# Kernel tuning notes

Hardware: AMD Instinct MI355X
Metric: run time of the kernel (lower is better)

## Reference

```python
import jax, jax.numpy as jnp
import numpy as np

N = 50000      # num nodes
E = 800000     # num edges (before self loops)
HID = 64       # hidden_channels
HEADS = 4
B = 256        # num graphs in batch
TEXT, VIS, AUD = 768, 512, 128


def setup_inputs() -> dict:
    key = jax.random.key(0)
    ks = jax.random.split(key, 24)
    rn = lambda k, shape: jax.random.normal(k, shape, dtype=jnp.float32) * 0.05
    inp = {}
    inp["x"] = jax.random.normal(ks[0], (N, TEXT), dtype=jnp.float32)
    inp["node_type"] = jax.random.randint(ks[1], (N,), 0, 3, dtype=jnp.int32)
    inp["edge_index"] = jax.random.randint(ks[2], (2, E), 0, N, dtype=jnp.int32)
    inp["batch"] = jnp.sort(jax.random.randint(ks[3], (N,), 0, B, dtype=jnp.int32))
    # modality projections
    inp["Wt"] = rn(ks[4], (TEXT, HID)); inp["bt"] = jnp.zeros((HID,), jnp.float32)
    inp["Wv"] = rn(ks[5], (VIS, HID));  inp["bv"] = jnp.zeros((HID,), jnp.float32)
    inp["Wa"] = rn(ks[6], (AUD, HID));  inp["ba"] = jnp.zeros((HID,), jnp.float32)
    # GATConv1: in=HID, out=HID, heads=HEADS, concat=True
    inp["W1"]  = rn(ks[7], (HID, HEADS * HID))
    inp["a1s"] = rn(ks[8], (HEADS, HID))
    inp["a1d"] = rn(ks[9], (HEADS, HID))
    inp["b1"]  = jnp.zeros((HEADS * HID,), jnp.float32)
    # GATConv2: in=HID*HEADS, out=HID, heads=1, concat=False
    inp["W2"]  = rn(ks[10], (HID * HEADS, HID))
    inp["a2s"] = rn(ks[11], (1, HID))
    inp["a2d"] = rn(ks[12], (1, HID))
    inp["b2"]  = jnp.zeros((HID,), jnp.float32)
    # final classifier (num_classes==2 -> out_dim 1, squeezed)
    inp["Wl"] = rn(ks[13], (HID, 1)); inp["bl"] = jnp.zeros((1,), jnp.float32)
    return inp


def gat_conv(x, edge_index, W, a_src, a_dst, bias, concat):
    """PyG-style GATConv (eval mode, add_self_loops=True, shared lin for src/dst)."""
    n = x.shape[0]
    heads, c = a_src.shape
    loops = jnp.arange(n, dtype=edge_index.dtype)
    src = jnp.concatenate([edge_index[0], loops])
    dst = jnp.concatenate([edge_index[1], loops])
    h = (x @ W).reshape(n, heads, c)                       # [N, H, C]
    alpha_s = jnp.einsum('nhc,hc->nh', h, a_src)           # [N, H]
    alpha_d = jnp.einsum('nhc,hc->nh', h, a_dst)
    e = jax.nn.leaky_relu(alpha_s[src] + alpha_d[dst], 0.2)  # [E', H]
    # numerically-stable softmax over incoming edges of each dst node
    m = jax.ops.segment_max(e, dst, num_segments=n)
    e = jnp.exp(e - m[dst])
    denom = jax.ops.segment_sum(e, dst, num_segments=n)
    alpha = e / (denom[dst] + 1e-16)                        # [E', H]
    out = jax.ops.segment_sum(h[src] * alpha[:, :, None], dst, num_segments=n)
    out = out.reshape(n, heads * c) if concat else out.mean(axis=1)
    return out + bias


def reference(x, node_type, edge_index, batch,
              Wt, bt, Wv, bv, Wa, ba,
              W1, a1s, a1d, b1, W2, a2s, a2d, b2, Wl, bl):
    # masked multimodal projection (type 0=text, 1=vision, 2=audio)
    t = x[:, :TEXT] @ Wt + bt
    v = x[:, :VIS] @ Wv + bv
    a = x[:, :AUD] @ Wa + ba
    nt = node_type[:, None]
    h = jnp.where(nt == 0, t, jnp.where(nt == 1, v, a))     # [N, HID]
    h = jax.nn.elu(gat_conv(h, edge_index, W1, a1s, a1d, b1, concat=True))
    h = gat_conv(h, edge_index, W2, a2s, a2d, b2, concat=False)  # [N, HID]
    # global mean pool over graphs
    sums = jax.ops.segment_sum(h, batch, num_segments=B)
    cnts = jax.ops.segment_sum(jnp.ones((h.shape[0], 1), h.dtype), batch, num_segments=B)
    g = sums / jnp.maximum(cnts, 1.0)                       # [B, HID]
    out = (g @ Wl + bl).squeeze(-1)                          # [B] (binary logit)
    return out
```

## Files before the change

### kernel.cpp

```cpp
#include <hip/hip_runtime.h>
#include <cstdint>
#include <cstddef>

#define TEXTD 768
#define VISD  512
#define AUDD  128

__device__ __forceinline__ float wred_sum(float v){
  #pragma unroll
  for (int m = 32; m >= 1; m >>= 1) v += __shfl_xor(v, m, 64);
  return v;
}
__device__ __forceinline__ float wred_max(float v){
  #pragma unroll
  for (int m = 32; m >= 1; m >>= 1) v = fmaxf(v, __shfl_xor(v, m, 64));
  return v;
}

__global__ __launch_bounds__(256) void k_bcount(const int* __restrict__ ntype, int nN, int nblk,
                                                int* __restrict__ bcnt){
  int b = blockIdx.x;
  int i = b*256 + threadIdx.x;
  int lane = threadIdx.x & 63, w = threadIdx.x >> 6;
  int ty = (i < nN) ? ntype[i] : -1;
  __shared__ int wc[4][3];
  #pragma unroll
  for (int t = 0; t < 3; t++){
    unsigned long long m = __ballot(ty == t);
    if (lane == 0) wc[w][t] = __popcll(m);
  }
  __syncthreads();
  if (threadIdx.x < 3){
    int t = threadIdx.x;
    bcnt[t*nblk + b] = wc[0][t] + wc[1][t] + wc[2][t] + wc[3][t];
  }
}
__global__ __launch_bounds__(1024) void k_bscan(const int* __restrict__ bcnt, int nblk, int nN,
                                                int* __restrict__ boff, int* __restrict__ toff,
                                                int* __restrict__ tcnt){
  __shared__ int s[2048];
  int n3 = nblk*3;
  int t = threadIdx.x;
  for (int i = t; i < n3; i += 1024) s[i] = bcnt[i];
  __syncthreads();
  if (t == 0){
    int run = 0;
    for (int i = 0; i < n3; i++){ int v = s[i]; s[i] = run; run += v; }
  }
  __syncthreads();
  for (int i = t; i < n3; i += 1024) boff[i] = s[i];
  if (t == 0){
    toff[0] = 0;         toff[1] = s[nblk];           toff[2] = s[2*nblk];
    tcnt[0] = s[nblk];   tcnt[1] = s[2*nblk]-s[nblk]; tcnt[2] = nN - s[2*nblk];
  }
}
__global__ __launch_bounds__(256) void k_bscatter(const int* __restrict__ ntype, int nN, int nblk,
                                                  const int* __restrict__ boff, int* __restrict__ order){
  int b = blockIdx.x;
  int i = b*256 + threadIdx.x;
  int lane = threadIdx.x & 63, w = threadIdx.x >> 6;
  int ty = (i < nN) ? ntype[i] : -1;
  __shared__ int wc[4][3];
  __shared__ int woff[4][3];
  unsigned long long masks[3];
  #pragma unroll
  for (int t = 0; t < 3; t++){
    masks[t] = __ballot(ty == t);
    if (lane == 0) wc[w][t] = __popcll(masks[t]);
  }
  __syncthreads();
  if (threadIdx.x < 3){
    int t = threadIdx.x, run = 0;
    #pragma unroll
    for (int ww = 0; ww < 4; ww++){ woff[ww][t] = run; run += wc[ww][t]; }
  }
  __syncthreads();
  if (ty >= 0){
    int r = __popcll(masks[ty] & ((1ULL << lane) - 1ULL));
    int pos = boff[ty*nblk + b] + woff[w][ty] + r;
    order[pos] = i;
  }
}

__global__ __launch_bounds__(256) void k_projgemm(const float* __restrict__ x,
    const int* __restrict__ order, const int* __restrict__ toff, const int* __restrict__ tcnt,
    const float* __restrict__ Wt, const float* __restrict__ bt,
    const float* __restrict__ Wv, const float* __restrict__ bv,
    const float* __restrict__ Wa, const float* __restrict__ ba,
    float* __restrict__ h0){
  int ty = blockIdx.y;
  int cnt = tcnt[ty];
  int tile = blockIdx.x;
  if (tile*64 >= cnt) return;
  const float* W; const float* bias; int dim;
  if (ty == 0)      { W = Wt; bias = bt; dim = TEXTD; }
  else if (ty == 1) { W = Wv; bias = bv; dim = VISD; }
  else              { W = Wa; bias = ba; dim = AUDD; }
  int off = toff[ty];

  __shared__ float xsT[64][68];
  __shared__ float ws [64][68];
  __shared__ int   nid[64];

  int t = threadIdx.x;
  if (t < 64){
    int idx = tile*64 + t;
    nid[t] = (idx < cnt) ? order[off + idx] : -1;
  }
  __syncthreads();

  int node_l = t & 63;
  int ndl = nid[node_l];
  const float* xrow = x + (size_t)(ndl < 0 ? 0 : ndl) * TEXTD;
  int wrow = t >> 2, wu = t & 3;
  int wvq  = t >> 6;
  int n0 = (t & 15)*4, c0 = (t >> 4)*4;
  float acc[4][4] = {};

  for (int k0 = 0; k0 < dim; k0 += 64){
    __syncthreads();
    #pragma unroll
    for (int j = 0; j < 4; j++){
      int f4 = wvq*4 + j;
      float4 v = *reinterpret_cast<const float4*>(xrow + k0 + f4*4);
      xsT[f4*4+0][node_l] = v.x;
      xsT[f4*4+1][node_l] = v.y;
      xsT[f4*4+2][node_l] = v.z;
      xsT[f4*4+3][node_l] = v.w;
    }
    #pragma unroll
    for (int j = 0; j < 4; j++){
      int f4 = j*4 + wu;
      float4 v = *reinterpret_cast<const float4*>(W + (size_t)(k0 + wrow)*64 + f4*4);
      *reinterpret_cast<float4*>(&ws[wrow][f4*4]) = v;
    }
    __syncthreads();
    #pragma unroll 8
    for (int kk = 0; kk < 64; kk++){
      float4 xv = *reinterpret_cast<const float4*>(&xsT[kk][n0]);
      float4 wv = *reinterpret_cast<const float4*>(&ws[kk][c0]);
      float xa[4] = {xv.x, xv.y, xv.z, xv.w};
      float wb[4] = {wv.x, wv.y, wv.z, wv.w};
      #pragma unroll
      for (int i = 0; i < 4; i++)
        #pragma unroll
        for (int j = 0; j < 4; j++)
          acc[i][j] += xa[i] * wb[j];
    }
  }

  float4 b4 = *reinterpret_cast<const float4*>(bias + c0);
  float bb[4] = {b4.x, b4.y, b4.z, b4.w};
  #pragma unroll
  for (int i = 0; i < 4; i++){
    int nd = nid[n0 + i];
    if (nd >= 0){
      float4 o4 = make_float4(acc[i][0]+bb[0], acc[i][1]+bb[1], acc[i][2]+bb[2], acc[i][3]+bb[3]);
      *reinterpret_cast<float4*>(h0 + (size_t)nd*64 + c0) = o4;
    }
  }
}

__global__ void k_deg_init(int* __restrict__ deg, int nN){
  int i = blockIdx.x*blockDim.x + threadIdx.x;
  if (i < nN) deg[i] = 1;
}
__global__ void k_deg_edges(const int* __restrict__ ei, int E, int* __restrict__ deg){
  int i = blockIdx.x*blockDim.x + threadIdx.x;
  if (i < E) atomicAdd(&deg[ei[E + i]], 1);
}
__global__ __launch_bounds__(1024) void k_scan(const int* __restrict__ deg, int* __restrict__ off, int n){
  __shared__ int wsum[16];
  __shared__ int carry_s;
  int t = threadIdx.x, lane = t & 63, w = t >> 6;
  if (t == 0) carry_s = 0;
  __syncthreads();
  for (int base = 0; base < n; base += 1024){
    int i = base + t;
    int v = (i < n) ? deg[i] : 0;
    int orig = v;
    #pragma unroll
    for (int o = 1; o < 64; o <<= 1){ int u = __shfl_up(v, o, 64); if (lane >= o) v += u; }
    if (lane == 63) wsum[w] = v;
    __syncthreads();
    if (t < 16){
      int xv = wsum[t];
      #pragma unroll
      for (int o = 1; o < 16; o <<= 1){ int u = __shfl_up(xv, o, 16); if (t >= o) xv += u; }
      wsum[t] = xv;
    }
    __syncthreads();
    int wbase = (w == 0) ? 0 : wsum[w-1];
    int incl = v + wbase;
    int carry = carry_s;
    if (i < n) off[i] = carry + incl - orig;
    __syncthreads();
    if (t == 0) carry_s = carry + wsum[15];
    __syncthreads();
  }
  if (threadIdx.x == 0) off[n] = carry_s;
}
__global__ void k_pos_copy(const int* __restrict__ off, int* __restrict__ pos, int nN){
  int i = blockIdx.x*blockDim.x + threadIdx.x;
  if (i < nN) pos[i] = off[i];
}
__global__ void k_scatter(const int* __restrict__ ei, int E, int nN,
                          int* __restrict__ pos, int* __restrict__ csr_src){
  int i = blockIdx.x*blockDim.x + threadIdx.x;
  int total = E + nN;
  if (i >= total) return;
  int s, d;
  if (i < E){ s = ei[i]; d = ei[E + i]; } else { s = i - E; d = s; }
  int p = atomicAdd(&pos[d], 1);
  csr_src[p] = s;
}

__global__ __launch_bounds__(256) void k_afold(const float* __restrict__ W1,
    const float* __restrict__ a1s, const float* __restrict__ a1d,
    float* __restrict__ wfs, float* __restrict__ wfd){
  int t = threadIdx.x;
  int k = t & 63, h = t >> 6;
  const float* wr = W1 + (size_t)k*256 + h*64;
  const float* as = a1s + h*64;
  const float* ad = a1d + h*64;
  float s = 0.f, d = 0.f;
  for (int c = 0; c < 64; c += 4){
    float4 w  = *reinterpret_cast<const float4*>(wr + c);
    float4 sa = *reinterpret_cast<const float4*>(as + c);
    float4 da = *reinterpret_cast<const float4*>(ad + c);
    s += w.x*sa.x + w.y*sa.y + w.z*sa.z + w.w*sa.w;
    d += w.x*da.x + w.y*da.y + w.z*da.z + w.w*da.w;
  }
  wfs[k*4 + h] = s;
  wfd[k*4 + h] = d;
}

__global__ __launch_bounds__(256) void k_alpha1(const float* __restrict__ h0,
    const float* __restrict__ wfs, const float* __restrict__ wfd,
    float* __restrict__ as1, float* __restrict__ ad1, int nN){
  __shared__ float xsT[64][68];
  __shared__ float sW[64][8];
  int t = threadIdx.x;
  int base = blockIdx.x*64;
  int row = t >> 2, fq = t & 3;
  {
    int nd = base + row; if (nd >= nN) nd = nN - 1;
    const float* hr = h0 + (size_t)nd*64;
    #pragma unroll
    for (int j = 0; j < 4; j++){
      int f4 = j*4 + fq;
      float4 v = *reinterpret_cast<const float4*>(hr + f4*4);
      xsT[f4*4+0][row] = v.x; xsT[f4*4+1][row] = v.y;
      xsT[f4*4+2][row] = v.z; xsT[f4*4+3][row] = v.w;
    }
  }
  if (t < 64){
    float4 s4 = *reinterpret_cast<const float4*>(wfs + t*4);
    float4 d4 = *reinterpret_cast<const float4*>(wfd + t*4);
    sW[t][0]=s4.x; sW[t][1]=s4.y; sW[t][2]=s4.z; sW[t][3]=s4.w;
    sW[t][4]=d4.x; sW[t][5]=d4.y; sW[t][6]=d4.z; sW[t][7]=d4.w;
  }
  __syncthreads();
  int node = t >> 2, h = t & 3;
  float s = 0.f, d = 0.f;
  #pragma unroll 8
  for (int k = 0; k < 64; k++){
    float xv = xsT[k][node];
    s += xv * sW[k][h];
    d += xv * sW[k][h+4];
  }
  int nd = base + node;
  if (nd < nN){ as1[nd*4 + h] = s; ad1[nd*4 + h] = d; }
}

__global__ __launch_bounds__(64) void k_gat1z(const int* __restrict__ off, const int* __restrict__ srcs,
    const float* __restrict__ as1, const float* __restrict__ ad1,
    const float* __restrict__ h0, float* __restrict__ z, int nN){
  int n = blockIdx.x;
  int L = threadIdx.x;
  int hL = L >> 4, c4 = (L & 15)*4;
  __shared__ int   s_src[64];
  __shared__ float s_p[64][4];
  float ad[4];
  { float4 a = *reinterpret_cast<const float4*>(ad1 + (size_t)n*4);
    ad[0]=a.x; ad[1]=a.y; ad[2]=a.z; ad[3]=a.w; }
  int s0 = off[n], s1 = off[n+1];
  float m[4] = {-1e30f,-1e30f,-1e30f,-1e30f};
  float den[4] = {0.f,0.f,0.f,0.f};
  float4 acc = make_float4(0.f,0.f,0.f,0.f);
  for (int base = s0; base < s1; base += 64){
    int e = base + L;
    int cl = min(64, s1 - base);
    bool valid = (e < s1);
    int sv = 0; float v[4];
    if (valid){
      sv = srcs[e];
      float4 a = *reinterpret_cast<const float4*>(as1 + (size_t)sv*4);
      float av[4] = {a.x,a.y,a.z,a.w};
      #pragma unroll
      for (int h = 0; h < 4; h++){ float tt = av[h] + ad[h]; v[h] = (tt>0.f)?tt:0.2f*tt; }
    } else {
      #pragma unroll
      for (int h = 0; h < 4; h++) v[h] = -1e30f;
    }
    float sc[4];
    #pragma unroll
    for (int h = 0; h < 4; h++){
      float cm = wred_max(v[h]);
      float mn = fmaxf(m[h], cm);
      sc[h] = __expf(m[h] - mn);
      m[h] = mn;
      float p = valid ? __expf(v[h] - mn) : 0.f;
      den[h] = den[h]*sc[h] + wred_sum(p);
      if (valid) s_p[L][h] = p;
    }
    { float s4 = sc[hL]; acc.x*=s4; acc.y*=s4; acc.z*=s4; acc.w*=s4; }
    if (valid) s_src[L] = sv;
    __syncthreads();
    #pragma unroll 4
    for (int e2 = 0; e2 < cl; e2++){
      int sr = s_src[e2];
      float pp = s_p[e2][hL];
      float4 hv = *reinterpret_cast<const float4*>(h0 + (size_t)sr*64 + c4);
      acc.x += pp*hv.x; acc.y += pp*hv.y; acc.z += pp*hv.z; acc.w += pp*hv.w;
    }
    __syncthreads();
  }
  float dl = den[hL] + 1e-16f;
  *reinterpret_cast<float4*>(z + (size_t)n*256 + hL*64 + c4) =
      make_float4(acc.x/dl, acc.y/dl, acc.z/dl, acc.w/dl);
}

__global__ __launch_bounds__(256) void k_glin1(const float* __restrict__ z,
    const float* __restrict__ W1, const float* __restrict__ b1,
    float* __restrict__ g1, int nN){
  int tile = blockIdx.x, q = blockIdx.y;
  int base = tile*64;
  __shared__ float xsT[64][68];
  __shared__ float ws [64][68];
  int t = threadIdx.x;
  int row = t >> 2, fq = t & 3;
  {
    int nd = base + row; if (nd >= nN) nd = nN - 1;
    const float* zr = z + (size_t)nd*256 + q*64;
    #pragma unroll
    for (int j = 0; j < 4; j++){
      int f4 = j*4 + fq;
      float4 v = *reinterpret_cast<const float4*>(zr + f4*4);
      xsT[f4*4+0][row] = v.x; xsT[f4*4+1][row] = v.y;
      xsT[f4*4+2][row] = v.z; xsT[f4*4+3][row] = v.w;
    }
  }
  #pragma unroll
  for (int j = 0; j < 4; j++){
    int f4 = j*4 + fq;
    float4 v = *reinterpret_cast<const float4*>(W1 + (size_t)row*256 + q*64 + f4*4);
    *reinterpret_cast<float4*>(&ws[row][f4*4]) = v;
  }
  __syncthreads();

  int n0 = (t & 15)*4, c0 = (t >> 4)*4;
  float acc[4][4] = {};
  #pragma unroll 8
  for (int k = 0; k < 64; k++){
    float4 xv = *reinterpret_cast<const float4*>(&xsT[k][n0]);
    float4 wv = *reinterpret_cast<const float4*>(&ws[k][c0]);
    float xa[4] = {xv.x, xv.y, xv.z, xv.w};
    float wb[4] = {wv.x, wv.y, wv.z, wv.w};
    #pragma unroll
    for (int i = 0; i < 4; i++)
      #pragma unroll
      for (int j = 0; j < 4; j++)
        acc[i][j] += xa[i] * wb[j];
  }
  float4 b4 = *reinterpret_cast<const float4*>(b1 + q*64 + c0);
  float bb[4] = {b4.x, b4.y, b4.z, b4.w};
  #pragma unroll
  for (int i = 0; i < 4; i++){
    int nd = base + n0 + i;
    if (nd < nN){
      float o[4];
      #pragma unroll
      for (int j = 0; j < 4; j++){
        float u = acc[i][j] + bb[j];
        o[j] = (u > 0.f) ? u : expm1f(u);
      }
      *reinterpret_cast<float4*>(g1 + (size_t)nd*256 + q*64 + c0) =
          make_float4(o[0], o[1], o[2], o[3]);
    }
  }
}

__global__ __launch_bounds__(256) void k_lin2t(const float* __restrict__ g1,
    const float* __restrict__ W2, const float* __restrict__ a2s, const float* __restrict__ a2d,
    float* __restrict__ h2, float* __restrict__ as2, float* __restrict__ ad2, int nN){
  int tile = blockIdx.x;
  int base = tile*64;
  __shared__ float xsT[64][68];
  __shared__ float ws [64][68];
  __shared__ float sPart[16][64];
  __shared__ float dPart[16][64];

  int t = threadIdx.x;
  int row = t >> 2, fq = t & 3;
  int ndl = base + row; if (ndl >= nN) ndl = nN - 1;
  const float* gr = g1 + (size_t)ndl*256;
  int n0 = (t & 15)*4, c0 = (t >> 4)*4, qg = t >> 4;
  float acc[4][4] = {};

  for (int k0 = 0; k0 < 256; k0 += 64){
    __syncthreads();
    #pragma unroll
    for (int j = 0; j < 4; j++){
      int f4 = j*4 + fq;
      float4 v = *reinterpret_cast<const float4*>(gr + k0 + f4*4);
      xsT[f4*4+0][row] = v.x; xsT[f4*4+1][row] = v.y;
      xsT[f4*4+2][row] = v.z; xsT[f4*4+3][row] = v.w;
    }
    #pragma unroll
    for (int j = 0; j < 4; j++){
      int f4 = j*4 + fq;
      float4 v = *reinterpret_cast<const float4*>(W2 + (size_t)(k0 + row)*64 + f4*4);
      *reinterpret_cast<float4*>(&ws[row][f4*4]) = v;
    }
    __syncthreads();
    #pragma unroll 8
    for (int k = 0; k < 64; k++){
      float4 xv = *reinterpret_cast<const float4*>(&xsT[k][n0]);
      float4 wv = *reinterpret_cast<const float4*>(&ws[k][c0]);
      float xa[4] = {xv.x, xv.y, xv.z, xv.w};
      float wb[4] = {wv.x, wv.y, wv.z, wv.w};
      #pragma unroll
      for (int i = 0; i < 4; i++)
        #pragma unroll
        for (int j = 0; j < 4; j++)
          acc[i][j] += xa[i] * wb[j];
    }
  }

  float avs[4], avd[4];
  {
    float4 s4 = *reinterpret_cast<const float4*>(a2s + c0);
    float4 d4 = *reinterpret_cast<const float4*>(a2d + c0);
    avs[0]=s4.x; avs[1]=s4.y; avs[2]=s4.z; avs[3]=s4.w;
    avd[0]=d4.x; avd[1]=d4.y; avd[2]=d4.z; avd[3]=d4.w;
  }
  #pragma unroll
  for (int i = 0; i < 4; i++){
    int nd = base + n0 + i;
    float sp = acc[i][0]*avs[0] + acc[i][1]*avs[1] + acc[i][2]*avs[2] + acc[i][3]*avs[3];
    float dp = acc[i][0]*avd[0] + acc[i][1]*avd[1] + acc[i][2]*avd[2] + acc[i][3]*avd[3];
    sPart[qg][n0+i] = sp;
    dPart[qg][n0+i] = dp;
    if (nd < nN){
      float4 o4 = make_float4(acc[i][0], acc[i][1], acc[i][2], acc[i][3]);
      *reinterpret_cast<float4*>(h2 + (size_t)nd*64 + c0) = o4;
    }
  }
  __syncthreads();
  if (t < 64){
    int nd = base + t;
    if (nd < nN){
      float s = 0.f, d = 0.f;
      #pragma unroll
      for (int g = 0; g < 16; g++){ s += sPart[g][t]; d += dPart[g][t]; }
      as2[nd] = s;
      ad2[nd] = d;
    }
  }
}

__global__ __launch_bounds__(256) void k_gat2v(const int* __restrict__ off, const int* __restrict__ srcs,
    const float* __restrict__ as2, const float* __restrict__ ad2,
    const float* __restrict__ h2, const float* __restrict__ b2,
    float* __restrict__ g2, int nN){
  int w = threadIdx.x >> 6, L = threadIdx.x & 63;
  int n = blockIdx.x*4 + w;
  if (n >= nN) return;
  int g = L >> 4, c4 = (L & 15)*4;
  float ad = ad2[n];
  int s0 = off[n], s1 = off[n+1];
  float m = -1e30f, den = 0.f;
  float4 acc = make_float4(0.f,0.f,0.f,0.f);
  for (int base = s0; base < s1; base += 64){
    int e = base + L;
    int cl = min(64, s1 - base);
    bool valid = (e < s1);
    int sv = 0; float v = -1e30f;
    if (valid){
      sv = srcs[e];
      float tt = as2[sv] + ad;
      v = (tt>0.f)?tt:0.2f*tt;
    }
    float cm = wred_max(v);
    float mn = fmaxf(m, cm);
    float sc = __expf(m - mn);
    m = mn;
    float p = valid ? __expf(v - mn) : 0.f;
    den = den*sc + wred_sum(p);
    acc.x*=sc; acc.y*=sc; acc.z*=sc; acc.w*=sc;
    int iters = (cl + 3) >> 2;
    for (int it = 0; it < iters; ++it){
      int e2   = it*4 + g;
      int esrc = (e2 < cl) ? e2 : (cl - 1);
      int   sr = __shfl(sv, esrc, 64);
      float pp = __shfl(p,  esrc, 64);
      if (e2 < cl){
        float4 hv = *reinterpret_cast<const float4*>(h2 + (size_t)sr*64 + c4);
        acc.x += pp*hv.x; acc.y += pp*hv.y; acc.z += pp*hv.z; acc.w += pp*hv.w;
      }
    }
  }
  #pragma unroll
  for (int s = 16; s <= 32; s <<= 1){
    acc.x += __shfl_xor(acc.x, s, 64);
    acc.y += __shfl_xor(acc.y, s, 64);
    acc.z += __shfl_xor(acc.z, s, 64);
    acc.w += __shfl_xor(acc.w, s, 64);
  }
  float dl = den + 1e-16f;
  if (L < 16){
    float4 b4 = *reinterpret_cast<const float4*>(b2 + c4);
    float4 o4 = make_float4(acc.x/dl + b4.x, acc.y/dl + b4.y,
                            acc.z/dl + b4.z, acc.w/dl + b4.w);
    *reinterpret_cast<float4*>(g2 + (size_t)n*64 + c4) = o4;
  }
}

__global__ void k_bstart(const int* __restrict__ batch, int nN, int B, int* __restrict__ bstart){
  int i = blockIdx.x*blockDim.x + threadIdx.x;
  if (i < nN){
    int prev = (i == 0) ? -1 : batch[i-1];
    int cur  = batch[i];
    for (int b = prev+1; b <= cur; b++) bstart[b] = i;
  } else if (i == nN){
    int last = batch[nN-1];
    for (int b = last+1; b <= B; b++) bstart[b] = nN;
  }
}

__global__ __launch_bounds__(64) void k_pool(const float* __restrict__ g2, const int* __restrict__ bstart,
    const float* __restrict__ Wl, const float* __restrict__ bl, float* __restrict__ out, int B){
  int b = blockIdx.x, c = threadIdx.x;
  int r0 = bstart[b], r1 = bstart[b+1];
  float s = 0.f;
  int i = r0;
  for (; i + 4 <= r1; i += 4){
    s += g2[(size_t)(i+0)*64 + c];
    s += g2[(size_t)(i+1)*64 + c];
    s += g2[(size_t)(i+2)*64 + c];
    s += g2[(size_t)(i+3)*64 + c];
  }
  for (; i < r1; i++) s += g2[(size_t)i*64 + c];
  float g = s / fmaxf((float)(r1 - r0), 1.f);
  float v = wred_sum(g * Wl[c]);
  if (c == 0) out[b] = v + bl[0];
}

extern "C" void kernel_launch(void* const* d_in, const int* in_sizes, int n_in,
                              void* d_out, int out_size, void* d_ws, size_t ws_size,
                              hipStream_t stream){
  const float* x    = (const float*)d_in[0];
  const int*   ntyp = (const int*)  d_in[1];
  const int*   ei   = (const int*)  d_in[2];
  const int*   batch= (const int*)  d_in[3];
  const float* Wt = (const float*)d_in[4];
  const float* bt = (const float*)d_in[5];
  const float* Wv = (const float*)d_in[6];
  const float* bv = (const float*)d_in[7];
  const float* Wa = (const float*)d_in[8];
  const float* ba = (const float*)d_in[9];
  const float* W1 = (const float*)d_in[10];
  const float* a1s= (const float*)d_in[11];
  const float* a1d= (const float*)d_in[12];
  const float* b1 = (const float*)d_in[13];
  const float* W2 = (const float*)d_in[14];
  const float* a2s= (const float*)d_in[15];
  const float* a2d= (const float*)d_in[16];
  const float* b2 = (const float*)d_in[17];
  const float* Wl = (const float*)d_in[18];
  const float* bl = (const float*)d_in[19];

  const int N = in_sizes[1];
  const int E = in_sizes[2] / 2;
  const int B = out_size;
  const int nblk = (N + 255)/256;

  char* ws = (char*)d_ws;
  size_t o = 0;
  auto alloc = [&](size_t bytes) -> void* {
    void* p = ws + o;
    o = (o + bytes + 255) & ~(size_t)255;
    return p;
  };
  int*   csr_off = (int*)  alloc((size_t)(N+1)*4);
  int*   pos     = (int*)  alloc((size_t)N*4);
  int*   csr_src = (int*)  alloc((size_t)(E+N)*4);
  float* as1     = (float*)alloc((size_t)N*4*4);
  float* ad1     = (float*)alloc((size_t)N*4*4);
  float* h0      = (float*)alloc((size_t)N*64*4);
  float* zbuf    = (float*)alloc((size_t)N*256*4);
  float* g1      = (float*)alloc((size_t)N*256*4);
  int*   bstart  = (int*)  alloc((size_t)(B+1)*4);
  int*   bcnt    = (int*)  alloc((size_t)nblk*3*4);
  int*   boff    = (int*)  alloc((size_t)nblk*3*4);
  int*   toff    = (int*)  alloc(3*4);
  int*   tcnt    = (int*)  alloc(3*4);
  int*   order   = (int*)  alloc((size_t)N*4);
  float* wfs     = (float*)alloc(256*4);
  float* wfd     = (float*)alloc(256*4);
  float* h2  = h0;
  float* as2 = as1;
  float* ad2 = ad1;
  float* g2  = zbuf;

  k_bcount  <<<nblk, 256, 0, stream>>>(ntyp, N, nblk, bcnt);
  k_bscan   <<<1, 1024, 0, stream>>>(bcnt, nblk, N, boff, toff, tcnt);
  k_bscatter<<<nblk, 256, 0, stream>>>(ntyp, N, nblk, boff, order);

  k_deg_init <<<(N + 255)/256, 256, 0, stream>>>(pos, N);
  k_deg_edges<<<(E + 255)/256, 256, 0, stream>>>(ei, E, pos);
  k_scan     <<<1, 1024, 0, stream>>>(pos, csr_off, N);
  k_pos_copy <<<(N + 255)/256, 256, 0, stream>>>(csr_off, pos, N);
  k_scatter  <<<(E + N + 255)/256, 256, 0, stream>>>(ei, E, N, pos, csr_src);

  k_bstart<<<(N + 1 + 255)/256, 256, 0, stream>>>(batch, N, B, bstart);

  k_afold<<<1, 256, 0, stream>>>(W1, a1s, a1d, wfs, wfd);

  {
    dim3 g((N + 63)/64, 3);
    k_projgemm<<<g, 256, 0, stream>>>(x, order, toff, tcnt, Wt, bt, Wv, bv, Wa, ba, h0);
  }

  k_alpha1<<<(N + 63)/64, 256, 0, stream>>>(h0, wfs, wfd, as1, ad1, N);
  k_gat1z <<<N, 64, 0, stream>>>(csr_off, csr_src, as1, ad1, h0, zbuf, N);
  {
    dim3 g((N + 63)/64, 4);
    k_glin1<<<g, 256, 0, stream>>>(zbuf, W1, b1, g1, N);
  }

  k_lin2t<<<(N + 63)/64, 256, 0, stream>>>(g1, W2, a2s, a2d, h2, as2, ad2, N);
  k_gat2v<<<(N + 3)/4, 256, 0, stream>>>(csr_off, csr_src, as2, ad2, h2, b2, g2, N);
  k_pool<<<B, 64, 0, stream>>>(g2, bstart, Wl, bl, (float*)d_out, B);
}
```

Measured before the change: 386.6 us.

## Fuse attention logits into projection GEMM, merge setup kernels, batch GAT1 nodes per block

Computes layer-1 source and destination attention logits in the projection GEMM epilogue, using a shared-memory partial reduction, so the separate k_alpha1 pass and its reread of h0 go away. Degree initialisation moves into k_bcount, and the scan now writes the scatter cursor directly, which removes two small kernel launches. k_gat1z now processes four nodes per 256-thread block, one wavefront per node, with per-wave shared buffers and no block barriers. The wave-local shared-memory handoff relies on wavefront lockstep execution, and the GEMM epilogue adds shared-memory traffic and a serial 64-thread reduction.

```diff
diff --git a/kernel.cpp b/kernel.cpp
--- a/kernel.cpp
+++ b/kernel.cpp
@@ -18,11 +18,12 @@
 }
 
 __global__ __launch_bounds__(256) void k_bcount(const int* __restrict__ ntype, int nN, int nblk,
-                                                int* __restrict__ bcnt){
+                                                int* __restrict__ bcnt, int* __restrict__ deg){
   int b = blockIdx.x;
   int i = b*256 + threadIdx.x;
   int lane = threadIdx.x & 63, w = threadIdx.x >> 6;
   int ty = (i < nN) ? ntype[i] : -1;
+  if (i < nN) deg[i] = 1;
   __shared__ int wc[4][3];
   #pragma unroll
   for (int t = 0; t < 3; t++){
@@ -82,94 +83,11 @@
   }
 }
 
-__global__ __launch_bounds__(256) void k_projgemm(const float* __restrict__ x,
-    const int* __restrict__ order, const int* __restrict__ toff, const int* __restrict__ tcnt,
-    const float* __restrict__ Wt, const float* __restrict__ bt,
-    const float* __restrict__ Wv, const float* __restrict__ bv,
-    const float* __restrict__ Wa, const float* __restrict__ ba,
-    float* __restrict__ h0){
-  int ty = blockIdx.y;
-  int cnt = tcnt[ty];
-  int tile = blockIdx.x;
-  if (tile*64 >= cnt) return;
-  const float* W; const float* bias; int dim;
-  if (ty == 0)      { W = Wt; bias = bt; dim = TEXTD; }
-  else if (ty == 1) { W = Wv; bias = bv; dim = VISD; }
-  else              { W = Wa; bias = ba; dim = AUDD; }
-  int off = toff[ty];
-
-  __shared__ float xsT[64][68];
-  __shared__ float ws [64][68];
-  __shared__ int   nid[64];
-
-  int t = threadIdx.x;
-  if (t < 64){
-    int idx = tile*64 + t;
-    nid[t] = (idx < cnt) ? order[off + idx] : -1;
-  }
-  __syncthreads();
-
-  int node_l = t & 63;
-  int ndl = nid[node_l];
-  const float* xrow = x + (size_t)(ndl < 0 ? 0 : ndl) * TEXTD;
-  int wrow = t >> 2, wu = t & 3;
-  int wvq  = t >> 6;
-  int n0 = (t & 15)*4, c0 = (t >> 4)*4;
-  float acc[4][4] = {};
-
-  for (int k0 = 0; k0 < dim; k0 += 64){
-    __syncthreads();
-    #pragma unroll
-    for (int j = 0; j < 4; j++){
-      int f4 = wvq*4 + j;
-      float4 v = *reinterpret_cast<const float4*>(xrow + k0 + f4*4);
-      xsT[f4*4+0][node_l] = v.x;
-      xsT[f4*4+1][node_l] = v.y;
-      xsT[f4*4+2][node_l] = v.z;
-      xsT[f4*4+3][node_l] = v.w;
-    }
-    #pragma unroll
-    for (int j = 0; j < 4; j++){
-      int f4 = j*4 + wu;
-      float4 v = *reinterpret_cast<const float4*>(W + (size_t)(k0 + wrow)*64 + f4*4);
-      *reinterpret_cast<float4*>(&ws[wrow][f4*4]) = v;
-    }
-    __syncthreads();
-    #pragma unroll 8
-    for (int kk = 0; kk < 64; kk++){
-      float4 xv = *reinterpret_cast<const float4*>(&xsT[kk][n0]);
-      float4 wv = *reinterpret_cast<const float4*>(&ws[kk][c0]);
-      float xa[4] = {xv.x, xv.y, xv.z, xv.w};
-      float wb[4] = {wv.x, wv.y, wv.z, wv.w};
-      #pragma unroll
-      for (int i = 0; i < 4; i++)
-        #pragma unroll
-        for (int j = 0; j < 4; j++)
-          acc[i][j] += xa[i] * wb[j];
-    }
-  }
-
-  float4 b4 = *reinterpret_cast<const float4*>(bias + c0);
-  float bb[4] = {b4.x, b4.y, b4.z, b4.w};
-  #pragma unroll
-  for (int i = 0; i < 4; i++){
-    int nd = nid[n0 + i];
-    if (nd >= 0){
-      float4 o4 = make_float4(acc[i][0]+bb[0], acc[i][1]+bb[1], acc[i][2]+bb[2], acc[i][3]+bb[3]);
-      *reinterpret_cast<float4*>(h0 + (size_t)nd*64 + c0) = o4;
-    }
-  }
-}
-
-__global__ void k_deg_init(int* __restrict__ deg, int nN){
-  int i = blockIdx.x*blockDim.x + threadIdx.x;
-  if (i < nN) deg[i] = 1;
-}
 __global__ void k_deg_edges(const int* __restrict__ ei, int E, int* __restrict__ deg){
   int i = blockIdx.x*blockDim.x + threadIdx.x;
   if (i < E) atomicAdd(&deg[ei[E + i]], 1);
 }
-__global__ __launch_bounds__(1024) void k_scan(const int* __restrict__ deg, int* __restrict__ off, int n){
+__global__ __launch_bounds__(1024) void k_scan(int* __restrict__ deg, int* __restrict__ off, int n){
   __shared__ int wsum[16];
   __shared__ int carry_s;
   int t = threadIdx.x, lane = t & 63, w = t >> 6;
@@ -193,16 +111,12 @@
     int wbase = (w == 0) ? 0 : wsum[w-1];
     int incl = v + wbase;
     int carry = carry_s;
-    if (i < n) off[i] = carry + incl - orig;
+    if (i < n){ int e = carry + incl - orig; off[i] = e; deg[i] = e; }
     __syncthreads();
     if (t == 0) carry_s = carry + wsum[15];
     __syncthreads();
   }
   if (threadIdx.x == 0) off[n] = carry_s;
-}
-__global__ void k_pos_copy(const int* __restrict__ off, int* __restrict__ pos, int nN){
-  int i = blockIdx.x*blockDim.x + threadIdx.x;
-  if (i < nN) pos[i] = off[i];
 }
 __global__ void k_scatter(const int* __restrict__ ei, int E, int nN,
                           int* __restrict__ pos, int* __restrict__ csr_src){
@@ -235,52 +149,139 @@
   wfd[k*4 + h] = d;
 }
 
-__global__ __launch_bounds__(256) void k_alpha1(const float* __restrict__ h0,
+__global__ __launch_bounds__(256) void k_projgemm(const float* __restrict__ x,
+    const int* __restrict__ order, const int* __restrict__ toff, const int* __restrict__ tcnt,
+    const float* __restrict__ Wt, const float* __restrict__ bt,
+    const float* __restrict__ Wv, const float* __restrict__ bv,
+    const float* __restrict__ Wa, const float* __restrict__ ba,
     const float* __restrict__ wfs, const float* __restrict__ wfd,
-    float* __restrict__ as1, float* __restrict__ ad1, int nN){
+    float* __restrict__ h0, float* __restrict__ as1, float* __restrict__ ad1){
+  int ty = blockIdx.y;
+  int cnt = tcnt[ty];
+  int tile = blockIdx.x;
+  if (tile*64 >= cnt) return;
+  const float* W; const float* bias; int dim;
+  if (ty == 0)      { W = Wt; bias = bt; dim = TEXTD; }
+  else if (ty == 1) { W = Wv; bias = bv; dim = VISD; }
+  else              { W = Wa; bias = ba; dim = AUDD; }
+  int off = toff[ty];
+
   __shared__ float xsT[64][68];
-  __shared__ float sW[64][8];
+  __shared__ float ws [64][68];
+  __shared__ int   nid[64];
+
   int t = threadIdx.x;
-  int base = blockIdx.x*64;
-  int row = t >> 2, fq = t & 3;
-  {
-    int nd = base + row; if (nd >= nN) nd = nN - 1;
-    const float* hr = h0 + (size_t)nd*64;
+  if (t < 64){
+    int idx = tile*64 + t;
+    nid[t] = (idx < cnt) ? order[off + idx] : -1;
+  }
+  __syncthreads();
+
+  int node_l = t & 63;
+  int ndl = nid[node_l];
+  const float* xrow = x + (size_t)(ndl < 0 ? 0 : ndl) * TEXTD;
+  int wrow = t >> 2, wu = t & 3;
+  int wvq  = t >> 6;
+  int n0 = (t & 15)*4, c0 = (t >> 4)*4, qg = t >> 4;
+  float acc[4][4] = {};
+
+  for (int k0 = 0; k0 < dim; k0 += 64){
+    __syncthreads();
     #pragma unroll
     for (int j = 0; j < 4; j++){
-      int f4 = j*4 + fq;
-      float4 v = *reinterpret_cast<const float4*>(hr + f4*4);
-      xsT[f4*4+0][row] = v.x; xsT[f4*4+1][row] = v.y;
-      xsT[f4*4+2][row] = v.z; xsT[f4*4+3][row] = v.w;
-    }
-  }
+      int f4 = wvq*4 + j;
+      float4 v = *reinterpret_cast<const float4*>(xrow + k0 + f4*4);
+      xsT[f4*4+0][node_l] = v.x;
+      xsT[f4*4+1][node_l] = v.y;
+      xsT[f4*4+2][node_l] = v.z;
+      xsT[f4*4+3][node_l] = v.w;
+    }
+    #pragma unroll
+    for (int j = 0; j < 4; j++){
+      int f4 = j*4 + wu;
+      float4 v = *reinterpret_cast<const float4*>(W + (size_t)(k0 + wrow)*64 + f4*4);
+      *reinterpret_cast<float4*>(&ws[wrow][f4*4]) = v;
+    }
+    __syncthreads();
+    #pragma unroll 8
+    for (int kk = 0; kk < 64; kk++){
+      float4 xv = *reinterpret_cast<const float4*>(&xsT[kk][n0]);
+      float4 wv = *reinterpret_cast<const float4*>(&ws[kk][c0]);
+      float xa[4] = {xv.x, xv.y, xv.z, xv.w};
+      float wb[4] = {wv.x, wv.y, wv.z, wv.w};
+      #pragma unroll
+      for (int i = 0; i < 4; i++)
+        #pragma unroll
+        for (int j = 0; j < 4; j++)
+          acc[i][j] += xa[i] * wb[j];
+    }
+  }
+
+  float4 b4 = *reinterpret_cast<const float4*>(bias + c0);
+  float bb[4] = {b4.x, b4.y, b4.z, b4.w};
+  #pragma unroll
+  for (int i = 0; i < 4; i++){
+    int nd = nid[n0 + i];
+    if (nd >= 0){
+      float4 o4 = make_float4(acc[i][0]+bb[0], acc[i][1]+bb[1], acc[i][2]+bb[2], acc[i][3]+bb[3]);
+      *reinterpret_cast<float4*>(h0 + (size_t)nd*64 + c0) = o4;
+    }
+  }
+
+  __syncthreads();
+  float* spart = &ws [0][0];
+  float* dpart = &xsT[0][0];
+  float4 wsv[4], wdv[4];
+  #pragma unroll
+  for (int j = 0; j < 4; j++){
+    wsv[j] = *reinterpret_cast<const float4*>(wfs + (c0+j)*4);
+    wdv[j] = *reinterpret_cast<const float4*>(wfd + (c0+j)*4);
+  }
+  #pragma unroll
+  for (int i = 0; i < 4; i++){
+    float hv[4];
+    #pragma unroll
+    for (int j = 0; j < 4; j++) hv[j] = acc[i][j] + bb[j];
+    float s0v = hv[0]*wsv[0].x + hv[1]*wsv[1].x + hv[2]*wsv[2].x + hv[3]*wsv[3].x;
+    float s1v = hv[0]*wsv[0].y + hv[1]*wsv[1].y + hv[2]*wsv[2].y + hv[3]*wsv[3].y;
+    float s2v = hv[0]*wsv[0].z + hv[1]*wsv[1].z + hv[2]*wsv[2].z + hv[3]*wsv[3].z;
+    float s3v = hv[0]*wsv[0].w + hv[1]*wsv[1].w + hv[2]*wsv[2].w + hv[3]*wsv[3].w;
+    float d0v = hv[0]*wdv[0].x + hv[1]*wdv[1].x + hv[2]*wdv[2].x + hv[3]*wdv[3].x;
+    float d1v = hv[0]*wdv[0].y + hv[1]*wdv[1].y + hv[2]*wdv[2].y + hv[3]*wdv[3].y;
+    float d2v = hv[0]*wdv[0].z + hv[1]*wdv[1].z + hv[2]*wdv[2].z + hv[3]*wdv[3].z;
+    float d3v = hv[0]*wdv[0].w + hv[1]*wdv[1].w + hv[2]*wdv[2].w + hv[3]*wdv[3].w;
+    int nidx = (n0 + i)*64 + qg*4;
+    spart[nidx+0]=s0v; spart[nidx+1]=s1v; spart[nidx+2]=s2v; spart[nidx+3]=s3v;
+    dpart[nidx+0]=d0v; dpart[nidx+1]=d1v; dpart[nidx+2]=d2v; dpart[nidx+3]=d3v;
+  }
+  __syncthreads();
   if (t < 64){
-    float4 s4 = *reinterpret_cast<const float4*>(wfs + t*4);
-    float4 d4 = *reinterpret_cast<const float4*>(wfd + t*4);
-    sW[t][0]=s4.x; sW[t][1]=s4.y; sW[t][2]=s4.z; sW[t][3]=s4.w;
-    sW[t][4]=d4.x; sW[t][5]=d4.y; sW[t][6]=d4.z; sW[t][7]=d4.w;
-  }
-  __syncthreads();
-  int node = t >> 2, h = t & 3;
-  float s = 0.f, d = 0.f;
-  #pragma unroll 8
-  for (int k = 0; k < 64; k++){
-    float xv = xsT[k][node];
-    s += xv * sW[k][h];
-    d += xv * sW[k][h+4];
-  }
-  int nd = base + node;
-  if (nd < nN){ as1[nd*4 + h] = s; ad1[nd*4 + h] = d; }
-}
-
-__global__ __launch_bounds__(64) void k_gat1z(const int* __restrict__ off, const int* __restrict__ srcs,
+    int nd = nid[t];
+    if (nd >= 0){
+      float s[4] = {0,0,0,0}, d[4] = {0,0,0,0};
+      #pragma unroll
+      for (int g = 0; g < 16; g++){
+        #pragma unroll
+        for (int h = 0; h < 4; h++){
+          s[h] += spart[t*64 + g*4 + h];
+          d[h] += dpart[t*64 + g*4 + h];
+        }
+      }
+      *reinterpret_cast<float4*>(as1 + (size_t)nd*4) = make_float4(s[0],s[1],s[2],s[3]);
+      *reinterpret_cast<float4*>(ad1 + (size_t)nd*4) = make_float4(d[0],d[1],d[2],d[3]);
+    }
+  }
+}
+
+__global__ __launch_bounds__(256) void k_gat1z(const int* __restrict__ off, const int* __restrict__ srcs,
     const float* __restrict__ as1, const float* __restrict__ ad1,
     const float* __restrict__ h0, float* __restrict__ z, int nN){
-  int n = blockIdx.x;
-  int L = threadIdx.x;
+  int w = threadIdx.x >> 6, L = threadIdx.x & 63;
+  int n = blockIdx.x*4 + w;
+  __shared__ int   s_src[4][64];
+  __shared__ float s_p[4][64][4];
+  if (n >= nN) return;
   int hL = L >> 4, c4 = (L & 15)*4;
-  __shared__ int   s_src[64];
-  __shared__ float s_p[64][4];
   float ad[4];
   { float4 a = *reinterpret_cast<const float4*>(ad1 + (size_t)n*4);
     ad[0]=a.x; ad[1]=a.y; ad[2]=a.z; ad[3]=a.w; }
@@ -303,7 +304,7 @@
       #pragma unroll
       for (int h = 0; h < 4; h++) v[h] = -1e30f;
     }
-    float sc[4];
+    float sc[4], pv[4];
     #pragma unroll
     for (int h = 0; h < 4; h++){
       float cm = wred_max(v[h]);
@@ -312,19 +313,20 @@
       m[h] = mn;
       float p = valid ? __expf(v[h] - mn) : 0.f;
       den[h] = den[h]*sc[h] + wred_sum(p);
-      if (valid) s_p[L][h] = p;
+      pv[h] = p;
     }
     { float s4 = sc[hL]; acc.x*=s4; acc.y*=s4; acc.z*=s4; acc.w*=s4; }
-    if (valid) s_src[L] = sv;
-    __syncthreads();
+    if (valid){
+      s_src[w][L] = sv;
+      *reinterpret_cast<float4*>(&s_p[w][L][0]) = make_float4(pv[0],pv[1],pv[2],pv[3]);
+    }
     #pragma unroll 4
     for (int e2 = 0; e2 < cl; e2++){
-      int sr = s_src[e2];
-      float pp = s_p[e2][hL];
+      int sr = s_src[w][e2];
+      float pp = s_p[w][e2][hL];
       float4 hv = *reinterpret_cast<const float4*>(h0 + (size_t)sr*64 + c4);
       acc.x += pp*hv.x; acc.y += pp*hv.y; acc.z += pp*hv.z; acc.w += pp*hv.w;
     }
-    __syncthreads();
   }
   float dl = den[hL] + 1e-16f;
   *reinterpret_cast<float4*>(z + (size_t)n*256 + hL*64 + c4) =
@@ -614,14 +616,12 @@
   float* ad2 = ad1;
   float* g2  = zbuf;
 
-  k_bcount  <<<nblk, 256, 0, stream>>>(ntyp, N, nblk, bcnt);
+  k_bcount  <<<nblk, 256, 0, stream>>>(ntyp, N, nblk, bcnt, pos);
   k_bscan   <<<1, 1024, 0, stream>>>(bcnt, nblk, N, boff, toff, tcnt);
   k_bscatter<<<nblk, 256, 0, stream>>>(ntyp, N, nblk, boff, order);
 
-  k_deg_init <<<(N + 255)/256, 256, 0, stream>>>(pos, N);
   k_deg_edges<<<(E + 255)/256, 256, 0, stream>>>(ei, E, pos);
   k_scan     <<<1, 1024, 0, stream>>>(pos, csr_off, N);
-  k_pos_copy <<<(N + 255)/256, 256, 0, stream>>>(csr_off, pos, N);
   k_scatter  <<<(E + N + 255)/256, 256, 0, stream>>>(ei, E, N, pos, csr_src);
 
   k_bstart<<<(N + 1 + 255)/256, 256, 0, stream>>>(batch, N, B, bstart);
@@ -630,11 +630,11 @@
 
   {
     dim3 g((N + 63)/64, 3);
-    k_projgemm<<<g, 256, 0, stream>>>(x, order, toff, tcnt, Wt, bt, Wv, bv, Wa, ba, h0);
-  }
-
-  k_alpha1<<<(N + 63)/64, 256, 0, stream>>>(h0, wfs, wfd, as1, ad1, N);
-  k_gat1z <<<N, 64, 0, stream>>>(csr_off, csr_src, as1, ad1, h0, zbuf, N);
+    k_projgemm<<<g, 256, 0, stream>>>(x, order, toff, tcnt, Wt, bt, Wv, bv, Wa, ba,
+                                      wfs, wfd, h0, as1, ad1);
+  }
+
+  k_gat1z <<<(N + 3)/4, 256, 0, stream>>>(csr_off, csr_src, as1, ad1, h0, zbuf, N);
   {
     dim3 g((N + 63)/64, 4);
     k_glin1<<<g, 256, 0, stream>>>(zbuf, W1, b1, g1, N);
```

Result: no change. 390.7 us (+1.1%).
